# Performance work log

Measured on AMD Instinct MI355X. Metric: run time of the kernel, lower is better.

The kernel has to match this reference:

```python
import jax, jax.numpy as jnp
import numpy as np

B, N, D, H = 2, 2048, 128, 16  # batch, seq, per-head dim, heads
ALL = D * H


def setup_inputs() -> dict:
    key = jax.random.key(0)
    ks = jax.random.split(key, 12)
    s = 0.02
    x = jax.random.normal(ks[0], (B, N, D), dtype=jnp.float32)
    mask = jax.random.randint(ks[1], (B, N), 0, 2, dtype=jnp.int32)
    Wq = jax.random.normal(ks[2], (D, ALL), dtype=jnp.float32) * s
    bq = jnp.zeros((ALL,), dtype=jnp.float32)
    Wk = jax.random.normal(ks[3], (D, ALL), dtype=jnp.float32) * s
    bk = jnp.zeros((ALL,), dtype=jnp.float32)
    Wv = jax.random.normal(ks[4], (D, ALL), dtype=jnp.float32) * s
    bv = jnp.zeros((ALL,), dtype=jnp.float32)
    Wo = jax.random.normal(ks[5], (ALL, D), dtype=jnp.float32) * s
    bo = jnp.zeros((D,), dtype=jnp.float32)
    return {"x": x, "mask": mask, "Wq": Wq, "bq": bq, "Wk": Wk, "bk": bk,
            "Wv": Wv, "bv": bv, "Wo": Wo, "bo": bo}


def reference(x, mask, Wq, bq, Wk, bk, Wv, bv, Wo, bo):
    b, n, d = x.shape
    h = ALL // d
    # project and split heads: [b, n, h, d] -> [b, h, n, d]
    q = (x @ Wq + bq).reshape(b, n, h, d).transpose(0, 2, 1, 3)
    k = (x @ Wk + bk).reshape(b, n, h, d).transpose(0, 2, 1, 3)
    v = (x @ Wv + bv).reshape(b, n, h, d).transpose(0, 2, 1, 3)
    scores = jnp.einsum('bhqd,bhkd->bhqk', q, k) / jnp.sqrt(jnp.float32(d))
    # key mask: [b,1,1,n]
    scores = jnp.where(mask[:, None, None, :] == 0, -jnp.inf, scores)
    attn = jax.nn.softmax(scores, axis=-1)  # dropout p=0.0 -> identity
    out = jnp.einsum('bhqk,bhkd->bhqd', attn, v)
    # query mask: [b,1,n,1]
    out = jnp.where(mask[:, None, :, None] == 0, 0.0, out)
    out = out.transpose(0, 2, 1, 3).reshape(b, n, h * d)
    return out @ Wo + bo
```

## Files before the change

kernel.cpp:

```cpp
#include <hip/hip_runtime.h>
#include <hip/hip_bf16.h>

#define B_   2
#define N_   2048
#define D_   128
#define H_   16
#define ALL_ 2048
#define M_   (B_*N_)
#define BH_  (B_*H_)

typedef __bf16 bf16;
typedef __bf16 bf16x8 __attribute__((ext_vector_type(8)));
typedef __bf16 bf16x4 __attribute__((ext_vector_type(4)));
typedef float  floatx4 __attribute__((ext_vector_type(4)));

#define MFMA32K(a,b,c) __builtin_amdgcn_mfma_f32_16x16x32_bf16((a),(b),(c),0,0,0)

__device__ inline void load_lds16(const bf16* g, bf16* l) {
    __builtin_amdgcn_global_load_lds((const __attribute__((address_space(1))) void*)g,
                                     (__attribute__((address_space(3))) void*)l, 16, 0, 0);
}

#define WAITCNT_VM(n) ((0xF << 8) | (0x7 << 4) | (n))


__global__ __launch_bounds__(256) void prep_weights(const float* __restrict__ x,
                                                    const float* __restrict__ Wq,
                                                    const float* __restrict__ Wk,
                                                    const float* __restrict__ Wv,
                                                    const float* __restrict__ Wo,
                                                    const int* __restrict__ mask,
                                                    bf16* __restrict__ Wqf,
                                                    bf16* __restrict__ Wkf,
                                                    bf16* __restrict__ Wvf,
                                                    bf16* __restrict__ Wof,
                                                    bf16* __restrict__ xf,
                                                    float* __restrict__ mbias) {
    __shared__ bf16 pw[16896];
    int bid = blockIdx.x, t = threadIdx.x;
    int lane = t & 63, wave = t >> 6;
    int lrow = lane & 15, quad = lane >> 4;

    if (bid < 192) {
        int m = bid / 64, rest = bid % 64;
        int cg = rest >> 1, kh = rest & 1;
        const float* W = (m == 0) ? Wq : (m == 1) ? Wk : Wv;
        bf16* Wf       = (m == 0) ? Wqf : (m == 1) ? Wkf : Wvf;
        int slot = t & 15, rowb = t >> 4;
#pragma unroll
        for (int i = 0; i < 4; i++) {
            int rl_ = rowb + i * 16;
            float4 v = *(const float4*)(W + (size_t)(kh * 64 + rl_) * 2048 + cg * 64 + slot * 4);
            bf16x4 o; o[0]=(bf16)v.x; o[1]=(bf16)v.y; o[2]=(bf16)v.z; o[3]=(bf16)v.w;
            *(bf16x4*)(&pw[rl_ * 68 + slot * 4]) = o;
        }
        __syncthreads();
        int ctl = wave;
#pragma unroll
        for (int kfl = 0; kfl < 2; kfl++) {
            bf16x8 w;
#pragma unroll
            for (int j = 0; j < 8; j++) w[j] = pw[(kfl * 32 + quad * 8 + j) * 68 + ctl * 16 + lrow];
            *(bf16x8*)(Wf + (size_t)((cg * 4 + ctl) * 4 + kh * 2 + kfl) * 512 + lane * 8) = w;
        }
    } else if (bid < 224) {
        int idx = bid - 192;
        int kb16 = idx >> 1, ch = idx & 1;
        int k0 = kb16 * 128;
        int slot = t & 15, rowb = t >> 4;
#pragma unroll
        for (int i = 0; i < 8; i++) {
            int r = rowb + i * 16;
            float4 v = *(const float4*)(Wo + (size_t)(k0 + r) * 128 + ch * 64 + slot * 4);
            bf16x4 o; o[0]=(bf16)v.x; o[1]=(bf16)v.y; o[2]=(bf16)v.z; o[3]=(bf16)v.w;
            *(bf16x4*)(&pw[r * 68 + slot * 4]) = o;
        }
        __syncthreads();
        int ctl = wave;
        int ct = ch * 4 + ctl;
#pragma unroll
        for (int kfl = 0; kfl < 4; kfl++) {
            bf16x8 w;
#pragma unroll
            for (int j = 0; j < 8; j++)
                w[j] = pw[(kfl * 32 + ((j >> 2) << 4) + quad * 4 + (j & 3)) * 68 + ctl * 16 + lrow];
            *(bf16x8*)(Wof + (size_t)(ct * 64 + kb16 * 4 + kfl) * 512 + lane * 8) = w;
        }
    } else if (bid < 352) {
        int idx = bid - 224, r0 = idx * 32;
        int slot = t & 31, rowb = t >> 5;
#pragma unroll
        for (int i = 0; i < 4; i++) {
            int r = rowb + i * 8;
            float4 v = *(const float4*)(x + (size_t)(r0 + r) * 128 + slot * 4);
            bf16x4 o; o[0]=(bf16)v.x; o[1]=(bf16)v.y; o[2]=(bf16)v.z; o[3]=(bf16)v.w;
            *(bf16x4*)(&pw[r * 136 + slot * 4]) = o;
        }
        __syncthreads();
        int rtl = wave >> 1;
        int kf2 = (wave & 1) * 2;
#pragma unroll
        for (int kfl = 0; kfl < 2; kfl++) {
            int kf = kf2 + kfl;
            bf16x8 w = *(const bf16x8*)(&pw[(rtl * 16 + lrow) * 136 + kf * 32 + quad * 8]);
            *(bf16x8*)(xf + (size_t)((idx * 2 + rtl) * 4 + kf) * 512 + lane * 8) = w;
        }
    } else {
        int e = (bid - 352) * 256 + t;
        mbias[e] = mask[e] ? 0.0f : -43.2808512f;
    }
}

__global__ __launch_bounds__(256) void qkv_proj(const bf16* __restrict__ xf,
                                                const float* __restrict__ bq,
                                                const float* __restrict__ bk,
                                                const float* __restrict__ bv,
                                                const bf16* __restrict__ Wqf,
                                                const bf16* __restrict__ Wkf,
                                                const bf16* __restrict__ Wvf,
                                                bf16* __restrict__ Qf,
                                                bf16* __restrict__ Kf,
                                                bf16* __restrict__ Vf) {
    __shared__ bf16 tile[64][72];

    int z = blockIdx.z;
    const float* bias = (z == 0) ? bq : (z == 1) ? bk : bv;
    const bf16*  Wf   = (z == 0) ? Wqf : (z == 1) ? Wkf : Wvf;

    int tid = threadIdx.x;
    int wave = tid >> 6, lane = tid & 63;
    int lrow = lane & 15, quad = lane >> 4;
    int r0b = blockIdx.x * 64;
    int c0 = blockIdx.y * 64;
    int cg4 = c0 >> 4;

    int rt = (r0b >> 4) + wave;
    bf16x8 a[4];
#pragma unroll
    for (int kf = 0; kf < 4; kf++)
        a[kf] = *(const bf16x8*)(xf + (size_t)(rt * 4 + kf) * 512 + lane * 8);

    int bb = r0b >> 11;
    int h  = c0 >> 7;
    int bhw = bb * 16 + h;
    int tile16 = (r0b & 2047) >> 4;
    int kbt = (r0b & 2047) >> 6;
    floatx4 zero4 = {0.f, 0.f, 0.f, 0.f};

    floatx4 acc[4] = {zero4, zero4, zero4, zero4};
#pragma unroll
    for (int kf = 0; kf < 4; kf++) {
#pragma unroll
        for (int nf = 0; nf < 4; nf++) {
            bf16x8 b = *(const bf16x8*)(Wf + (size_t)((cg4 + nf) * 4 + kf) * 512 + lane * 8);
            acc[nf] = MFMA32K(a[kf], b, acc[nf]);
        }
    }

#pragma unroll
    for (int nf = 0; nf < 4; nf++) {
        int col = nf * 16 + lrow;
        float bvv = bias[c0 + col];
#pragma unroll
        for (int r = 0; r < 4; r++) {
            int row = wave * 16 + quad * 4 + r;
            bf16 val = (bf16)(acc[nf][r] + bvv);
            if (z < 2) tile[row][col] = val;
            else       tile[col][row] = val;
        }
    }
    __syncthreads();

    if (z < 2) {
        bf16* dst = (z == 0) ? Qf : Kf;
        int s = wave;
        int kfbase = (c0 & 127) >> 5;
        size_t fbase = ((size_t)bhw * 128 + tile16 + s) * 4 + kfbase;
#pragma unroll
        for (int kfl = 0; kfl < 2; kfl++) {
            bf16x8 w = *(const bf16x8*)(&tile[s * 16 + lrow][kfl * 32 + quad * 8]);
            *(bf16x8*)(dst + (fbase + kfl) * 512 + lane * 8) = w;
        }
    } else {
        int nfl = wave;
        int nfbase = (c0 & 127) >> 4;
        size_t fbase = (((size_t)bhw * 32 + kbt) * 8 + (nfbase + nfl)) * 2;
#pragma unroll
        for (int g = 0; g < 2; g++) {
            bf16x4 a0 = *(const bf16x4*)(&tile[nfl * 16 + lrow][g * 32 + quad * 4]);
            bf16x4 a1 = *(const bf16x4*)(&tile[nfl * 16 + lrow][g * 32 + 16 + quad * 4]);
            bf16x8 w;
            w[0]=a0[0]; w[1]=a0[1]; w[2]=a0[2]; w[3]=a0[3];
            w[4]=a1[0]; w[5]=a1[1]; w[6]=a1[2]; w[7]=a1[3];
            *(bf16x8*)(Vf + (fbase + g) * 512 + lane * 8) = w;
        }
    }
}

__global__ __launch_bounds__(256) void flash_attn(const bf16* __restrict__ Qf,
                                                  const bf16* __restrict__ Kf,
                                                  const bf16* __restrict__ Vf,
                                                  const float* __restrict__ mbias,
                                                  const int* __restrict__ mask,
                                                  bf16* __restrict__ ctxf) {
    __shared__ bf16 sm[36864];
    float* mbL = (float*)&sm[32768];

    int tid = threadIdx.x;
    int wave = tid >> 6, lane = tid & 63;
    int lrow = lane & 15, quad = lane >> 4;
    int bid = blockIdx.x;
    int xcd = bid & 7, seq = bid >> 3;
    int bh  = xcd * 4 + (seq >> 4);
    int qblk = seq & 15;
    int b  = bh >> 4;
    int q0 = qblk * 128 + wave * 32;

    const float* mbp = mbias + b * N_;
    const bf16* kbase = Kf + (size_t)bh * 32 * 8192;
    const bf16* vbase = Vf + (size_t)bh * 32 * 8192;

    bf16x8 qf[2][4];
#pragma unroll
    for (int u = 0; u < 2; u++)
#pragma unroll
        for (int kf = 0; kf < 4; kf++)
            qf[u][kf] = *(const bf16x8*)(Qf + (size_t)(((size_t)bh * 128 + (q0 >> 4) + u) * 4 + kf) * 512 + lane * 8);

    bf16x8 ones;
#pragma unroll
    for (int j = 0; j < 8; j++) ones[j] = (bf16)1.0f;

    floatx4 zero4 = {0.f, 0.f, 0.f, 0.f};
    floatx4 O[2][8];
#pragma unroll
    for (int u = 0; u < 2; u++)
#pragma unroll
        for (int nf = 0; nf < 8; nf++) O[u][nf] = zero4;
    floatx4 Oext[2] = {zero4, zero4};

    const float scale = 0.12751742f;

#pragma unroll
    for (int i = 0; i < 4; i++) {
        int seg = wave * 4 + i;
        load_lds16(kbase + seg * 512 + lane * 8, &sm[seg * 512]);
        load_lds16(vbase + seg * 512 + lane * 8, &sm[8192 + seg * 512]);
    }
#pragma unroll
    for (int i = 0; i < 2; i++) {
        int seg = wave * 2 + i;
        load_lds16((const bf16*)(mbp + seg * 256) + lane * 8, (bf16*)(mbL + seg * 256));
    }

    for (int kb = 0; kb < 32; kb++) {
        int cur = (kb & 1) << 14;

        __builtin_amdgcn_s_waitcnt(WAITCNT_VM(0));
        __builtin_amdgcn_s_barrier();

        if (kb < 31) {
            int nxt = cur ^ 16384;
            const bf16* ksrc = kbase + (size_t)(kb + 1) * 8192;
            const bf16* vsrc = vbase + (size_t)(kb + 1) * 8192;
#pragma unroll
            for (int i = 0; i < 4; i++) {
                int seg = wave * 4 + i;
                load_lds16(ksrc + seg * 512 + lane * 8, &sm[nxt + seg * 512]);
                load_lds16(vsrc + seg * 512 + lane * 8, &sm[nxt + 8192 + seg * 512]);
            }
        }

        bf16x8 pf[2][2];
#pragma unroll
        for (int s = 0; s < 4; s++) {
            floatx4 S0 = zero4, S1 = zero4;
#pragma unroll
            for (int kf = 0; kf < 4; kf++) {
                bf16x8 kfr = *(const bf16x8*)(&sm[cur + ((s * 4 + kf) * 64 + lane) * 8]);
                S0 = MFMA32K(kfr, qf[0][kf], S0);
                S1 = MFMA32K(kfr, qf[1][kf], S1);
            }
            float4 mb4 = *(const float4*)(mbL + kb * 64 + s * 16 + quad * 4);
            const float* mbr = (const float*)&mb4;
            int g = s >> 1, o = (s & 1) * 4;
#pragma unroll
            for (int r = 0; r < 4; r++) {
                float p0 = __builtin_amdgcn_exp2f(fmaf(S0[r], scale, mbr[r]));
                float p1 = __builtin_amdgcn_exp2f(fmaf(S1[r], scale, mbr[r]));
                pf[0][g][o + r] = (bf16)p0;
                pf[1][g][o + r] = (bf16)p1;
            }
        }

#pragma unroll
        for (int g = 0; g < 2; g++) {
            Oext[0] = MFMA32K(ones, pf[0][g], Oext[0]);
            Oext[1] = MFMA32K(ones, pf[1][g], Oext[1]);
        }

#pragma unroll
        for (int nf = 0; nf < 8; nf++) {
#pragma unroll
            for (int g = 0; g < 2; g++) {
                bf16x8 vfr = *(const bf16x8*)(&sm[cur + 8192 + ((nf * 2 + g) * 64 + lane) * 8]);
                O[0][nf] = MFMA32K(vfr, pf[0][g], O[0][nf]);
                O[1][nf] = MFMA32K(vfr, pf[1][g], O[1][nf]);
            }
        }
    }

    const int* mp = mask + b * N_;
    int h4 = (bh & 15) * 4;
    size_t qtb = (size_t)b * 128 + (q0 >> 4);
#pragma unroll
    for (int u = 0; u < 2; u++) {
        float lsum = Oext[u][0];
        int q = q0 + u * 16 + lrow;
        float rl = (mp[q] && lsum > 0.f) ? (1.0f / lsum) : 0.f;
#pragma unroll
        for (int g = 0; g < 4; g++) {
            bf16x8 w;
#pragma unroll
            for (int j = 0; j < 4; j++) {
                w[j]     = (bf16)(O[u][2 * g][j]     * rl);
                w[j + 4] = (bf16)(O[u][2 * g + 1][j] * rl);
            }
            *(bf16x8*)(ctxf + ((qtb + u) * 64 + h4 + g) * 512 + lane * 8) = w;
        }
    }
}

__global__ __launch_bounds__(128) void out_proj(const bf16* __restrict__ ctxf,
                                                const bf16* __restrict__ Wof,
                                                const float* __restrict__ bo,
                                                float* __restrict__ out) {
    __shared__ float red[512];
    int tid = threadIdx.x;
    int wave = tid >> 6, lane = tid & 63;
    int lrow = lane & 15, quad = lane >> 4;
    int qt = blockIdx.x;
    int ct = blockIdx.y * 2;
    int r0 = qt * 16, c0 = ct * 16;

    floatx4 zero4 = {0.f, 0.f, 0.f, 0.f};
    floatx4 acc[2] = {zero4, zero4};
    const bf16* ap = ctxf + ((size_t)qt * 64 + wave * 32) * 512 + lane * 8;
    const bf16* b0 = Wof + ((size_t)ct * 64 + wave * 32) * 512 + lane * 8;
    const bf16* b1 = b0 + (size_t)64 * 512;
#pragma unroll 4
    for (int kf = 0; kf < 32; kf++) {
        bf16x8 a  = *(const bf16x8*)(ap + (size_t)kf * 512);
        bf16x8 w0 = *(const bf16x8*)(b0 + (size_t)kf * 512);
        bf16x8 w1 = *(const bf16x8*)(b1 + (size_t)kf * 512);
        acc[0] = MFMA32K(a, w0, acc[0]);
        acc[1] = MFMA32K(a, w1, acc[1]);
    }
    if (wave == 1) {
#pragma unroll
        for (int nf = 0; nf < 2; nf++)
#pragma unroll
            for (int r = 0; r < 4; r++)
                red[nf * 256 + r * 64 + lane] = acc[nf][r];
    }
    __syncthreads();
    if (wave == 0) {
#pragma unroll
        for (int nf = 0; nf < 2; nf++) {
            int col = c0 + nf * 16 + lrow;
            float bv = bo[col];
#pragma unroll
            for (int r = 0; r < 4; r++) {
                int m = r0 + quad * 4 + r;
                out[(size_t)m * 128 + col] = acc[nf][r] + red[nf * 256 + r * 64 + lane] + bv;
            }
        }
    }
}

extern "C" void kernel_launch(void* const* d_in, const int* in_sizes, int n_in,
                              void* d_out, int out_size, void* d_ws, size_t ws_size,
                              hipStream_t stream) {
    const float* x    = (const float*)d_in[0];
    const int*   mask = (const int*)d_in[1];
    const float* Wq   = (const float*)d_in[2];
    const float* bq   = (const float*)d_in[3];
    const float* Wk   = (const float*)d_in[4];
    const float* bk   = (const float*)d_in[5];
    const float* Wv   = (const float*)d_in[6];
    const float* bv   = (const float*)d_in[7];
    const float* Wo   = (const float*)d_in[8];
    const float* bo   = (const float*)d_in[9];
    float* out = (float*)d_out;

    char* ws = (char*)d_ws;
    size_t off = 0;
    bf16* Wqf = (bf16*)(ws + off); off += (size_t)262144 * 2;
    bf16* Wkf = (bf16*)(ws + off); off += (size_t)262144 * 2;
    bf16* Wvf = (bf16*)(ws + off); off += (size_t)262144 * 2;
    bf16* Wof = (bf16*)(ws + off); off += (size_t)262144 * 2;
    bf16* xf  = (bf16*)(ws + off); off += (size_t)524288 * 2;
    size_t qkv_elems = (size_t)BH_ * N_ * 128;
    bf16* Qf  = (bf16*)(ws + off); off += qkv_elems * 2;
    bf16* Kf  = (bf16*)(ws + off); off += qkv_elems * 2;
    bf16* Vf  = (bf16*)(ws + off); off += qkv_elems * 2;
    bf16* ctxf = (bf16*)(ws + off); off += (size_t)M_ * ALL_ * 2;
    float* mbias = (float*)(ws + off); off += (size_t)B_ * N_ * 4;
    (void)ws_size; (void)in_sizes; (void)n_in; (void)out_size;

    prep_weights<<<368, 256, 0, stream>>>(x, Wq, Wk, Wv, Wo, mask,
                                          Wqf, Wkf, Wvf, Wof, xf, mbias);

    qkv_proj<<<dim3(64, 32, 3), 256, 0, stream>>>(xf, bq, bk, bv, Wqf, Wkf, Wvf,
                                                  Qf, Kf, Vf);

    flash_attn<<<512, 256, 0, stream>>>(Qf, Kf, Vf, mbias, mask, ctxf);

    out_proj<<<dim3(256, 4), 128, 0, stream>>>(ctxf, Wof, bo, out);
}
```

Baseline: 180.5 us.

## Halve attention key tile, add MFMA priority hints, restructure out_proj to full-width tiles

```diff
diff --git a/kernel.cpp b/kernel.cpp
--- a/kernel.cpp
+++ b/kernel.cpp
@@ -203,8 +203,8 @@
                                                   const float* __restrict__ mbias,
                                                   const int* __restrict__ mask,
                                                   bf16* __restrict__ ctxf) {
-    __shared__ bf16 sm[36864];
-    float* mbL = (float*)&sm[32768];
+    __shared__ bf16 sm[16384];
+    __shared__ float mbL[2048];
 
     int tid = threadIdx.x;
     int wave = tid >> 6, lane = tid & 63;
@@ -217,8 +217,8 @@
     int q0 = qblk * 128 + wave * 32;
 
     const float* mbp = mbias + b * N_;
-    const bf16* kbase = Kf + (size_t)bh * 32 * 8192;
-    const bf16* vbase = Vf + (size_t)bh * 32 * 8192;
+    const bf16* kbase = Kf + (size_t)bh * 262144;
+    const bf16* vbase = Vf + (size_t)bh * 262144;
 
     bf16x8 qf[2][4];
 #pragma unroll
@@ -242,10 +242,10 @@
     const float scale = 0.12751742f;
 
 #pragma unroll
-    for (int i = 0; i < 4; i++) {
-        int seg = wave * 4 + i;
-        load_lds16(kbase + seg * 512 + lane * 8, &sm[seg * 512]);
-        load_lds16(vbase + seg * 512 + lane * 8, &sm[8192 + seg * 512]);
+    for (int i = 0; i < 2; i++) {
+        int s = wave * 2 + i;
+        load_lds16(kbase + s * 512 + lane * 8, &sm[s * 512]);
+        load_lds16(vbase + s * 1024 + lane * 8, &sm[4096 + s * 512]);
     }
 #pragma unroll
     for (int i = 0; i < 2; i++) {
@@ -253,61 +253,60 @@
         load_lds16((const bf16*)(mbp + seg * 256) + lane * 8, (bf16*)(mbL + seg * 256));
     }
 
-    for (int kb = 0; kb < 32; kb++) {
-        int cur = (kb & 1) << 14;
+    for (int t = 0; t < 64; t++) {
+        int cur = (t & 1) << 13;
 
         __builtin_amdgcn_s_waitcnt(WAITCNT_VM(0));
         __builtin_amdgcn_s_barrier();
 
-        if (kb < 31) {
-            int nxt = cur ^ 16384;
-            const bf16* ksrc = kbase + (size_t)(kb + 1) * 8192;
-            const bf16* vsrc = vbase + (size_t)(kb + 1) * 8192;
-#pragma unroll
-            for (int i = 0; i < 4; i++) {
-                int seg = wave * 4 + i;
-                load_lds16(ksrc + seg * 512 + lane * 8, &sm[nxt + seg * 512]);
-                load_lds16(vsrc + seg * 512 + lane * 8, &sm[nxt + 8192 + seg * 512]);
+        if (t < 63) {
+            int nxt = cur ^ 8192;
+            int tn = t + 1;
+            const bf16* ksrc = kbase + (size_t)tn * 4096;
+            const bf16* vsrc = vbase + (size_t)(tn >> 1) * 8192 + (size_t)(tn & 1) * 512;
+#pragma unroll
+            for (int i = 0; i < 2; i++) {
+                int s = wave * 2 + i;
+                load_lds16(ksrc + s * 512 + lane * 8, &sm[nxt + s * 512]);
+                load_lds16(vsrc + s * 1024 + lane * 8, &sm[nxt + 4096 + s * 512]);
             }
         }
 
-        bf16x8 pf[2][2];
-#pragma unroll
-        for (int s = 0; s < 4; s++) {
+        bf16x8 pf[2];
+#pragma unroll
+        for (int s = 0; s < 2; s++) {
             floatx4 S0 = zero4, S1 = zero4;
+            __builtin_amdgcn_s_setprio(1);
 #pragma unroll
             for (int kf = 0; kf < 4; kf++) {
                 bf16x8 kfr = *(const bf16x8*)(&sm[cur + ((s * 4 + kf) * 64 + lane) * 8]);
                 S0 = MFMA32K(kfr, qf[0][kf], S0);
                 S1 = MFMA32K(kfr, qf[1][kf], S1);
             }
-            float4 mb4 = *(const float4*)(mbL + kb * 64 + s * 16 + quad * 4);
+            __builtin_amdgcn_s_setprio(0);
+            float4 mb4 = *(const float4*)(mbL + t * 32 + s * 16 + quad * 4);
             const float* mbr = (const float*)&mb4;
-            int g = s >> 1, o = (s & 1) * 4;
+            int o = s * 4;
 #pragma unroll
             for (int r = 0; r < 4; r++) {
                 float p0 = __builtin_amdgcn_exp2f(fmaf(S0[r], scale, mbr[r]));
                 float p1 = __builtin_amdgcn_exp2f(fmaf(S1[r], scale, mbr[r]));
-                pf[0][g][o + r] = (bf16)p0;
-                pf[1][g][o + r] = (bf16)p1;
+                pf[0][o + r] = (bf16)p0;
+                pf[1][o + r] = (bf16)p1;
             }
         }
 
-#pragma unroll
-        for (int g = 0; g < 2; g++) {
-            Oext[0] = MFMA32K(ones, pf[0][g], Oext[0]);
-            Oext[1] = MFMA32K(ones, pf[1][g], Oext[1]);
-        }
-
+        Oext[0] = MFMA32K(ones, pf[0], Oext[0]);
+        Oext[1] = MFMA32K(ones, pf[1], Oext[1]);
+
+        __builtin_amdgcn_s_setprio(1);
 #pragma unroll
         for (int nf = 0; nf < 8; nf++) {
-#pragma unroll
-            for (int g = 0; g < 2; g++) {
-                bf16x8 vfr = *(const bf16x8*)(&sm[cur + 8192 + ((nf * 2 + g) * 64 + lane) * 8]);
-                O[0][nf] = MFMA32K(vfr, pf[0][g], O[0][nf]);
-                O[1][nf] = MFMA32K(vfr, pf[1][g], O[1][nf]);
-            }
-        }
+            bf16x8 vfr = *(const bf16x8*)(&sm[cur + 4096 + (nf * 64 + lane) * 8]);
+            O[0][nf] = MFMA32K(vfr, pf[0], O[0][nf]);
+            O[1][nf] = MFMA32K(vfr, pf[1], O[1][nf]);
+        }
+        __builtin_amdgcn_s_setprio(0);
     }
 
     const int* mp = mask + b * N_;
@@ -331,48 +330,51 @@
     }
 }
 
-__global__ __launch_bounds__(128) void out_proj(const bf16* __restrict__ ctxf,
+__global__ __launch_bounds__(256) void out_proj(const bf16* __restrict__ ctxf,
                                                 const bf16* __restrict__ Wof,
                                                 const float* __restrict__ bo,
                                                 float* __restrict__ out) {
-    __shared__ float red[512];
+    __shared__ float red[3 * 2048];
     int tid = threadIdx.x;
     int wave = tid >> 6, lane = tid & 63;
     int lrow = lane & 15, quad = lane >> 4;
     int qt = blockIdx.x;
-    int ct = blockIdx.y * 2;
-    int r0 = qt * 16, c0 = ct * 16;
 
     floatx4 zero4 = {0.f, 0.f, 0.f, 0.f};
-    floatx4 acc[2] = {zero4, zero4};
-    const bf16* ap = ctxf + ((size_t)qt * 64 + wave * 32) * 512 + lane * 8;
-    const bf16* b0 = Wof + ((size_t)ct * 64 + wave * 32) * 512 + lane * 8;
-    const bf16* b1 = b0 + (size_t)64 * 512;
+    floatx4 acc[8] = {zero4, zero4, zero4, zero4, zero4, zero4, zero4, zero4};
+    const bf16* ap = ctxf + ((size_t)qt * 64 + wave * 16) * 512 + lane * 8;
+    const bf16* bp = Wof + ((size_t)wave * 16) * 512 + lane * 8;
 #pragma unroll 4
-    for (int kf = 0; kf < 32; kf++) {
-        bf16x8 a  = *(const bf16x8*)(ap + (size_t)kf * 512);
-        bf16x8 w0 = *(const bf16x8*)(b0 + (size_t)kf * 512);
-        bf16x8 w1 = *(const bf16x8*)(b1 + (size_t)kf * 512);
-        acc[0] = MFMA32K(a, w0, acc[0]);
-        acc[1] = MFMA32K(a, w1, acc[1]);
-    }
-    if (wave == 1) {
-#pragma unroll
-        for (int nf = 0; nf < 2; nf++)
+    for (int kf = 0; kf < 16; kf++) {
+        bf16x8 a = *(const bf16x8*)(ap + (size_t)kf * 512);
+#pragma unroll
+        for (int ct = 0; ct < 8; ct++) {
+            bf16x8 w = *(const bf16x8*)(bp + ((size_t)ct * 64 + kf) * 512);
+            acc[ct] = MFMA32K(a, w, acc[ct]);
+        }
+    }
+    if (wave != 0) {
+#pragma unroll
+        for (int ct = 0; ct < 8; ct++)
 #pragma unroll
             for (int r = 0; r < 4; r++)
-                red[nf * 256 + r * 64 + lane] = acc[nf][r];
+                red[(wave - 1) * 2048 + ct * 256 + r * 64 + lane] = acc[ct][r];
     }
     __syncthreads();
     if (wave == 0) {
 #pragma unroll
-        for (int nf = 0; nf < 2; nf++) {
-            int col = c0 + nf * 16 + lrow;
+        for (int ct = 0; ct < 8; ct++) {
+            int col = ct * 16 + lrow;
             float bv = bo[col];
 #pragma unroll
             for (int r = 0; r < 4; r++) {
-                int m = r0 + quad * 4 + r;
-                out[(size_t)m * 128 + col] = acc[nf][r] + red[nf * 256 + r * 64 + lane] + bv;
+                int m = qt * 16 + quad * 4 + r;
+                float s = acc[ct][r]
+                        + red[0 * 2048 + ct * 256 + r * 64 + lane]
+                        + red[1 * 2048 + ct * 256 + r * 64 + lane]
+                        + red[2 * 2048 + ct * 256 + r * 64 + lane]
+                        + bv;
+                out[(size_t)m * 128 + col] = s;
             }
         }
     }
@@ -416,5 +418,5 @@
 
     flash_attn<<<512, 256, 0, stream>>>(Qf, Kf, Vf, mbias, mask, ctxf);
 
-    out_proj<<<dim3(256, 4), 128, 0, stream>>>(ctxf, Wof, bo, out);
-}
+    out_proj<<<256, 256, 0, stream>>>(ctxf, Wof, bo, out);
+}
```

Result: slower. 217.3 us (+20.4%).

## Load V fragments directly to registers and fuse QKV projections per block

Applied to the files above, without the earlier changes.

```diff
diff --git a/kernel.cpp b/kernel.cpp
--- a/kernel.cpp
+++ b/kernel.cpp
@@ -123,10 +123,6 @@
                                                 bf16* __restrict__ Vf) {
     __shared__ bf16 tile[64][72];
 
-    int z = blockIdx.z;
-    const float* bias = (z == 0) ? bq : (z == 1) ? bk : bv;
-    const bf16*  Wf   = (z == 0) ? Wqf : (z == 1) ? Wkf : Wvf;
-
     int tid = threadIdx.x;
     int wave = tid >> 6, lane = tid & 63;
     int lrow = lane & 15, quad = lane >> 4;
@@ -147,64 +143,71 @@
     int kbt = (r0b & 2047) >> 6;
     floatx4 zero4 = {0.f, 0.f, 0.f, 0.f};
 
-    floatx4 acc[4] = {zero4, zero4, zero4, zero4};
-#pragma unroll
-    for (int kf = 0; kf < 4; kf++) {
+#pragma unroll
+    for (int z = 0; z < 3; z++) {
+        const float* bias = (z == 0) ? bq : (z == 1) ? bk : bv;
+        const bf16*  Wf   = (z == 0) ? Wqf : (z == 1) ? Wkf : Wvf;
+
+        floatx4 acc[4] = {zero4, zero4, zero4, zero4};
+#pragma unroll
+        for (int kf = 0; kf < 4; kf++) {
+#pragma unroll
+            for (int nf = 0; nf < 4; nf++) {
+                bf16x8 b = *(const bf16x8*)(Wf + (size_t)((cg4 + nf) * 4 + kf) * 512 + lane * 8);
+                acc[nf] = MFMA32K(a[kf], b, acc[nf]);
+            }
+        }
+
 #pragma unroll
         for (int nf = 0; nf < 4; nf++) {
-            bf16x8 b = *(const bf16x8*)(Wf + (size_t)((cg4 + nf) * 4 + kf) * 512 + lane * 8);
-            acc[nf] = MFMA32K(a[kf], b, acc[nf]);
-        }
-    }
-
-#pragma unroll
-    for (int nf = 0; nf < 4; nf++) {
-        int col = nf * 16 + lrow;
-        float bvv = bias[c0 + col];
-#pragma unroll
-        for (int r = 0; r < 4; r++) {
-            int row = wave * 16 + quad * 4 + r;
-            bf16 val = (bf16)(acc[nf][r] + bvv);
-            if (z < 2) tile[row][col] = val;
-            else       tile[col][row] = val;
-        }
-    }
-    __syncthreads();
-
-    if (z < 2) {
-        bf16* dst = (z == 0) ? Qf : Kf;
-        int s = wave;
-        int kfbase = (c0 & 127) >> 5;
-        size_t fbase = ((size_t)bhw * 128 + tile16 + s) * 4 + kfbase;
-#pragma unroll
-        for (int kfl = 0; kfl < 2; kfl++) {
-            bf16x8 w = *(const bf16x8*)(&tile[s * 16 + lrow][kfl * 32 + quad * 8]);
-            *(bf16x8*)(dst + (fbase + kfl) * 512 + lane * 8) = w;
-        }
-    } else {
-        int nfl = wave;
-        int nfbase = (c0 & 127) >> 4;
-        size_t fbase = (((size_t)bhw * 32 + kbt) * 8 + (nfbase + nfl)) * 2;
-#pragma unroll
-        for (int g = 0; g < 2; g++) {
-            bf16x4 a0 = *(const bf16x4*)(&tile[nfl * 16 + lrow][g * 32 + quad * 4]);
-            bf16x4 a1 = *(const bf16x4*)(&tile[nfl * 16 + lrow][g * 32 + 16 + quad * 4]);
-            bf16x8 w;
-            w[0]=a0[0]; w[1]=a0[1]; w[2]=a0[2]; w[3]=a0[3];
-            w[4]=a1[0]; w[5]=a1[1]; w[6]=a1[2]; w[7]=a1[3];
-            *(bf16x8*)(Vf + (fbase + g) * 512 + lane * 8) = w;
-        }
-    }
-}
-
-__global__ __launch_bounds__(256) void flash_attn(const bf16* __restrict__ Qf,
-                                                  const bf16* __restrict__ Kf,
-                                                  const bf16* __restrict__ Vf,
-                                                  const float* __restrict__ mbias,
-                                                  const int* __restrict__ mask,
-                                                  bf16* __restrict__ ctxf) {
-    __shared__ bf16 sm[36864];
-    float* mbL = (float*)&sm[32768];
+            int col = nf * 16 + lrow;
+            float bvv = bias[c0 + col];
+#pragma unroll
+            for (int r = 0; r < 4; r++) {
+                int row = wave * 16 + quad * 4 + r;
+                bf16 val = (bf16)(acc[nf][r] + bvv);
+                if (z < 2) tile[row][col] = val;
+                else       tile[col][row] = val;
+            }
+        }
+        __syncthreads();
+
+        if (z < 2) {
+            bf16* dst = (z == 0) ? Qf : Kf;
+            int s = wave;
+            int kfbase = (c0 & 127) >> 5;
+            size_t fbase = ((size_t)bhw * 128 + tile16 + s) * 4 + kfbase;
+#pragma unroll
+            for (int kfl = 0; kfl < 2; kfl++) {
+                bf16x8 w = *(const bf16x8*)(&tile[s * 16 + lrow][kfl * 32 + quad * 8]);
+                *(bf16x8*)(dst + (fbase + kfl) * 512 + lane * 8) = w;
+            }
+        } else {
+            int nfl = wave;
+            int nfbase = (c0 & 127) >> 4;
+            size_t fbase = (((size_t)bhw * 32 + kbt) * 8 + (nfbase + nfl)) * 2;
+#pragma unroll
+            for (int g = 0; g < 2; g++) {
+                bf16x4 a0 = *(const bf16x4*)(&tile[nfl * 16 + lrow][g * 32 + quad * 4]);
+                bf16x4 a1 = *(const bf16x4*)(&tile[nfl * 16 + lrow][g * 32 + 16 + quad * 4]);
+                bf16x8 w;
+                w[0]=a0[0]; w[1]=a0[1]; w[2]=a0[2]; w[3]=a0[3];
+                w[4]=a1[0]; w[5]=a1[1]; w[6]=a1[2]; w[7]=a1[3];
+                *(bf16x8*)(Vf + (fbase + g) * 512 + lane * 8) = w;
+            }
+        }
+        if (z < 2) __syncthreads();
+    }
+}
+
+__global__ __launch_bounds__(256, 2) void flash_attn(const bf16* __restrict__ Qf,
+                                                     const bf16* __restrict__ Kf,
+                                                     const bf16* __restrict__ Vf,
+                                                     const float* __restrict__ mbias,
+                                                     const int* __restrict__ mask,
+                                                     bf16* __restrict__ ctxf) {
+    __shared__ bf16 sm[20480];
+    float* mbL = (float*)&sm[16384];
 
     int tid = threadIdx.x;
     int wave = tid >> 6, lane = tid & 63;
@@ -217,8 +220,8 @@
     int q0 = qblk * 128 + wave * 32;
 
     const float* mbp = mbias + b * N_;
-    const bf16* kbase = Kf + (size_t)bh * 32 * 8192;
-    const bf16* vbase = Vf + (size_t)bh * 32 * 8192;
+    const bf16* kbase = Kf + (size_t)bh * 262144;
+    const bf16* vbase = Vf + (size_t)bh * 262144;
 
     bf16x8 qf[2][4];
 #pragma unroll
@@ -245,7 +248,6 @@
     for (int i = 0; i < 4; i++) {
         int seg = wave * 4 + i;
         load_lds16(kbase + seg * 512 + lane * 8, &sm[seg * 512]);
-        load_lds16(vbase + seg * 512 + lane * 8, &sm[8192 + seg * 512]);
     }
 #pragma unroll
     for (int i = 0; i < 2; i++) {
@@ -254,33 +256,39 @@
     }
 
     for (int kb = 0; kb < 32; kb++) {
-        int cur = (kb & 1) << 14;
+        int cur = (kb & 1) << 13;
 
         __builtin_amdgcn_s_waitcnt(WAITCNT_VM(0));
         __builtin_amdgcn_s_barrier();
 
         if (kb < 31) {
-            int nxt = cur ^ 16384;
+            int nxt = cur ^ 8192;
             const bf16* ksrc = kbase + (size_t)(kb + 1) * 8192;
-            const bf16* vsrc = vbase + (size_t)(kb + 1) * 8192;
 #pragma unroll
             for (int i = 0; i < 4; i++) {
                 int seg = wave * 4 + i;
                 load_lds16(ksrc + seg * 512 + lane * 8, &sm[nxt + seg * 512]);
-                load_lds16(vsrc + seg * 512 + lane * 8, &sm[nxt + 8192 + seg * 512]);
-            }
-        }
+            }
+        }
+
+        const bf16* vsrc = vbase + (size_t)kb * 8192 + lane * 8;
+        bf16x8 vreg[16];
+#pragma unroll
+        for (int f = 0; f < 16; f++)
+            vreg[f] = *(const bf16x8*)(vsrc + f * 512);
 
         bf16x8 pf[2][2];
 #pragma unroll
         for (int s = 0; s < 4; s++) {
             floatx4 S0 = zero4, S1 = zero4;
+            __builtin_amdgcn_s_setprio(1);
 #pragma unroll
             for (int kf = 0; kf < 4; kf++) {
                 bf16x8 kfr = *(const bf16x8*)(&sm[cur + ((s * 4 + kf) * 64 + lane) * 8]);
                 S0 = MFMA32K(kfr, qf[0][kf], S0);
                 S1 = MFMA32K(kfr, qf[1][kf], S1);
             }
+            __builtin_amdgcn_s_setprio(0);
             float4 mb4 = *(const float4*)(mbL + kb * 64 + s * 16 + quad * 4);
             const float* mbr = (const float*)&mb4;
             int g = s >> 1, o = (s & 1) * 4;
@@ -299,15 +307,16 @@
             Oext[1] = MFMA32K(ones, pf[1][g], Oext[1]);
         }
 
+        __builtin_amdgcn_s_setprio(1);
 #pragma unroll
         for (int nf = 0; nf < 8; nf++) {
 #pragma unroll
             for (int g = 0; g < 2; g++) {
-                bf16x8 vfr = *(const bf16x8*)(&sm[cur + 8192 + ((nf * 2 + g) * 64 + lane) * 8]);
-                O[0][nf] = MFMA32K(vfr, pf[0][g], O[0][nf]);
-                O[1][nf] = MFMA32K(vfr, pf[1][g], O[1][nf]);
-            }
-        }
+                O[0][nf] = MFMA32K(vreg[nf * 2 + g], pf[0][g], O[0][nf]);
+                O[1][nf] = MFMA32K(vreg[nf * 2 + g], pf[1][g], O[1][nf]);
+            }
+        }
+        __builtin_amdgcn_s_setprio(0);
     }
 
     const int* mp = mask + b * N_;
@@ -411,8 +420,8 @@
     prep_weights<<<368, 256, 0, stream>>>(x, Wq, Wk, Wv, Wo, mask,
                                           Wqf, Wkf, Wvf, Wof, xf, mbias);
 
-    qkv_proj<<<dim3(64, 32, 3), 256, 0, stream>>>(xf, bq, bk, bv, Wqf, Wkf, Wvf,
-                                                  Qf, Kf, Vf);
+    qkv_proj<<<dim3(64, 32), 256, 0, stream>>>(xf, bq, bk, bv, Wqf, Wkf, Wvf,
+                                               Qf, Kf, Vf);
 
     flash_attn<<<512, 256, 0, stream>>>(Qf, Kf, Vf, mbias, mask, ctxf);
 
```

New measurement: 173.0 us. 4.2% less time.
